# Performance work log

Hardware: AMD Instinct MI355X
Metric: run time of the kernel (lower is better)

Reference implementation:

```python
import jax, jax.numpy as jnp
import numpy as np

SEQ_LEN = 12
BATCH = 2048
IN_DIM = 512
HIDDEN = 1024


def setup_inputs() -> dict:
    key = jax.random.key(0)
    k1, k2, k3, k4 = jax.random.split(key, 4)
    scale = 1.0 / np.sqrt(IN_DIM + HIDDEN)
    return {
        "x": jax.random.normal(k1, (BATCH, SEQ_LEN, IN_DIM), dtype=jnp.float32),
        "coded_cords": jax.random.normal(k2, (BATCH, HIDDEN), dtype=jnp.float32),
        # TF GRUCell fused gate kernel: [in+hidden, 2*hidden] (reset, update), bias init 1.0
        "gate_kernel": jax.random.normal(k3, (IN_DIM + HIDDEN, 2 * HIDDEN), dtype=jnp.float32) * scale,
        "gate_bias": jnp.ones((2 * HIDDEN,), dtype=jnp.float32),
        # candidate kernel: [in+hidden, hidden], zero bias
        "cand_kernel": jax.random.normal(k4, (IN_DIM + HIDDEN, HIDDEN), dtype=jnp.float32) * scale,
        "cand_bias": jnp.zeros((HIDDEN,), dtype=jnp.float32),
    }


def reference(x, coded_cords, gate_kernel, gate_bias, cand_kernel, cand_bias):
    # GRU recurrence (tf.contrib.rnn.GRUCell math), initial state = coded_cords.
    def step(h, xt):
        # xt: [B, D], h: [B, H]
        gates = jax.nn.sigmoid(jnp.concatenate([xt, h], axis=-1) @ gate_kernel + gate_bias)
        r, u = jnp.split(gates, 2, axis=-1)  # reset, update gates [B, H]
        c = jnp.tanh(jnp.concatenate([xt, r * h], axis=-1) @ cand_kernel + cand_bias)
        h_new = u * h + (1.0 - u) * c
        return h_new, h_new

    xs = jnp.swapaxes(x, 0, 1)  # [T, B, D]
    _, ys = jax.lax.scan(step, coded_cords, xs)  # ys: [T, B, H]
    return jnp.swapaxes(ys, 0, 1)  # [B, T, H]
```

## Files before the change

### kernel.cpp

```cpp
#include <hip/hip_runtime.h>
#include <hip/hip_bf16.h>


#define T_SEQ 12
#define BATCH 2048
#define IND 512
#define HID 1024
#define NGATE (2 * HID)
#define NPRE (NGATE + HID)

typedef __bf16 bf16x8 __attribute__((ext_vector_type(8)));
typedef __bf16 bf16x4 __attribute__((ext_vector_type(4)));
typedef float floatx4 __attribute__((ext_vector_type(4)));

#define AS1 __attribute__((address_space(1)))
#define AS3 __attribute__((address_space(3)))

__device__ __forceinline__ void gload16(const __bf16* g, __bf16* l) {
  __builtin_amdgcn_global_load_lds((const AS1 void*)g, (AS3 void*)l, 16, 0, 0);
}

__device__ __forceinline__ float fast_sigmoid(float v) {
  v = fminf(30.f, fmaxf(-30.f, v));
  return 1.f / (1.f + __expf(-v));
}
__device__ __forceinline__ float fast_tanh(float v) {
  v = fminf(15.f, fmaxf(-15.f, v));
  float e = __expf(2.f * v);
  return (e - 1.f) / (e + 1.f);
}

__global__ __launch_bounds__(256) void prep(
    const float* __restrict__ Wg, const float* __restrict__ Wc,
    const float* __restrict__ x, const float* __restrict__ coded,
    __bf16* __restrict__ Bx, __bf16* __restrict__ Bhg, __bf16* __restrict__ Bhc,
    __bf16* __restrict__ xb, float* __restrict__ h32, __bf16* __restrict__ hb) {
  int b = blockIdx.x;
  if (b < 2304) {
    int gid = b * 256 + threadIdx.x;
    int g = gid >> 6, lane = gid & 63;
    const float* W; int ld, row0, ksteps, wid; __bf16* out;
    if (g < 2048)      { W = Wg; ld = NGATE; row0 = 0;   ksteps = 16; wid = g;        out = Bx; }
    else if (g < 3072) { W = Wc; ld = HID;   row0 = 0;   ksteps = 16; wid = g - 2048; out = Bx + (size_t)2048 * 512; }
    else if (g < 7168) { W = Wg; ld = NGATE; row0 = IND; ksteps = 32; wid = g - 3072; out = Bhg; }
    else               { W = Wc; ld = HID;   row0 = IND; ksteps = 32; wid = g - 7168; out = Bhc; }
    int n16 = wid / ksteps, kt = wid - n16 * ksteps;
    int col = n16 * 16 + (lane & 15);
    int k0 = row0 + kt * 32 + (lane >> 4) * 8;
    bf16x8 v;
#pragma unroll
    for (int j = 0; j < 8; ++j) v[j] = (__bf16)W[(size_t)(k0 + j) * ld + col];
    *reinterpret_cast<bf16x8*>(out + (size_t)wid * 512 + lane * 8) = v;
  } else if (b < 4352) {
    int i = (b - 2304) * 256 + threadIdx.x;
    const float4* x4 = (const float4*)x;
    const int n4 = BATCH * T_SEQ * IND / 4;
    for (int k = i; k < n4; k += 2048 * 256) {
      float4 v = x4[k];
      bf16x4 o;
      o[0] = (__bf16)v.x; o[1] = (__bf16)v.y; o[2] = (__bf16)v.z; o[3] = (__bf16)v.w;
      *reinterpret_cast<bf16x4*>(xb + (size_t)k * 4) = o;
    }
  } else {
    int i = (b - 4352) * 256 + threadIdx.x;
    float4 v = ((const float4*)coded)[i];
    ((float4*)h32)[i] = v;
    bf16x4 o;
    o[0] = (__bf16)v.x; o[1] = (__bf16)v.y; o[2] = (__bf16)v.z; o[3] = (__bf16)v.w;
    *reinterpret_cast<bf16x4*>(hb + (size_t)i * 4) = o;
  }
}

__global__ __launch_bounds__(256) void pre_gemm(
    const __bf16* __restrict__ xb, const __bf16* __restrict__ Bx,
    const float* __restrict__ bg, const float* __restrict__ bc,
    __bf16* __restrict__ Pg, __bf16* __restrict__ Pc) {
  __shared__ __bf16 Alds[128 * 64];
  __shared__ __bf16 Blds[8192];
  const int tid = threadIdx.x, lane = tid & 63, w = tid >> 6;
  const int wm = w >> 1, wn = w & 1, quad = lane >> 4, l16 = lane & 15;
  const int bid = blockIdx.x;
  const int wg = (bid & 7) * 576 + (bid >> 3);
  const int nb = wg % 24;
  const int rest = wg / 24;
  const int mB = rest & 15;
  const int tz = rest >> 4;
  const int m0 = mB * 128;

  const __bf16* gA[4]; __bf16* lA[4];
  const __bf16* gB[4]; __bf16* lB[4];
#pragma unroll
  for (int i = 0; i < 4; ++i) {
    int c = tid + i * 256;
    int row = c >> 3, k8 = c & 7;
    gA[i] = xb + ((size_t)(m0 + row) * T_SEQ + tz) * IND + ((k8 ^ (row & 7)) * 8);
    lA[i] = Alds + c * 8;
    int ks2c = c >> 9, rem = c & 511;
    gB[i] = Bx + (((size_t)(nb * 8 + (rem >> 6)) * 16 + ks2c) * 64 + (rem & 63)) * 8;
    lB[i] = Blds + c * 8;
  }

  floatx4 acc[4][4] = {};
  for (int it = 0; it < 8; ++it) {
    __syncthreads();
#pragma unroll
    for (int i = 0; i < 4; ++i) gload16(gA[i] + it * 64, lA[i]);
#pragma unroll
    for (int i = 0; i < 4; ++i) gload16(gB[i] + (size_t)it * 1024, lB[i]);
    __syncthreads();
#pragma unroll
    for (int ks2 = 0; ks2 < 2; ++ks2) {
      bf16x8 af[4], bfr[4];
#pragma unroll
      for (int mf = 0; mf < 4; ++mf) {
        int row = wm * 64 + mf * 16 + l16;
        af[mf] = *(const bf16x8*)&Alds[row * 64 + (((ks2 * 4 + quad) ^ (row & 7)) * 8)];
      }
#pragma unroll
      for (int nf = 0; nf < 4; ++nf)
        bfr[nf] = *(const bf16x8*)&Blds[(ks2 * 512 + (wn * 4 + nf) * 64 + lane) * 8];
#pragma unroll
      for (int mf = 0; mf < 4; ++mf)
#pragma unroll
        for (int nf = 0; nf < 4; ++nf)
          acc[mf][nf] = __builtin_amdgcn_mfma_f32_16x16x32_bf16(af[mf], bfr[nf], acc[mf][nf], 0, 0, 0);
    }
  }

  const int n64g = nb * 2 + wn;
  const bool isg = (n64g < 32);
  __bf16* P = isg ? Pg : Pc;
  const float* bias = isg ? bg : bc;
  const int nrel = isg ? n64g : (n64g - 32);
  const int colb = nrel * 64 + l16;
#pragma unroll
  for (int mf = 0; mf < 4; ++mf) {
    int m32 = mB * 4 + wm * 2 + (mf >> 1);
    size_t tb = isg ? (((size_t)tz * 64 + m32) * 32 + n64g) * 2048
                    : (((size_t)tz * 64 + m32) * 16 + nrel) * 2048;
#pragma unroll
    for (int nf = 0; nf < 4; ++nf) {
      float bv = bias[colb + nf * 16];
      bf16x4 st;
#pragma unroll
      for (int i = 0; i < 4; ++i) st[i] = (__bf16)(acc[mf][nf][i] + bv);
      *(bf16x4*)&P[tb + (size_t)(((mf & 1) * 4 + nf) * 64 + lane) * 4] = st;
    }
  }
}

__global__ __launch_bounds__(256, 2) void gate_step(
    const __bf16* __restrict__ hb, const __bf16* __restrict__ Bhg,
    const __bf16* __restrict__ Pg, _Float16* __restrict__ u16,
    __bf16* __restrict__ rhb, int t) {
  __shared__ __bf16 Alds[64 * 128];
  __shared__ __bf16 Blds[16384];
  const int tid = threadIdx.x, lane = tid & 63, w = tid >> 6;
  const int wm = w >> 1, wn = w & 1, quad = lane >> 4, l16 = lane & 15;
  const int bid = blockIdx.x;
  const int swz = (bid & 7) * 64 + (bid >> 3);
  const int mT = swz & 31, nT = swz >> 5;

  const __bf16* gA[4]; __bf16* lA[4];
  const __bf16* gB[8]; __bf16* lB[8];
#pragma unroll
  for (int i = 0; i < 4; ++i) {
    int c = tid + i * 256;
    int row = c >> 4, ch = c & 15;
    gA[i] = hb + (size_t)(mT * 64 + row) * HID + ((ch ^ (row & 7)) * 8);
    lA[i] = Alds + c * 8;
  }
#pragma unroll
  for (int i = 0; i < 8; ++i) {
    int c = tid + i * 256;
    gB[i] = Bhg + (size_t)(nT * 8 + (c >> 8)) * 16384 + (c & 255) * 8;
    lB[i] = Blds + c * 8;
  }

  floatx4 acc[2][4] = {};
  for (int kt = 0; kt < 8; ++kt) {
    __syncthreads();
#pragma unroll
    for (int i = 0; i < 4; ++i) gload16(gA[i] + kt * 128, lA[i]);
#pragma unroll
    for (int i = 0; i < 8; ++i) gload16(gB[i] + kt * 2048, lB[i]);
    __syncthreads();
#pragma unroll
    for (int ks2 = 0; ks2 < 4; ++ks2) {
      bf16x8 af[2], bfr[4];
#pragma unroll
      for (int mf = 0; mf < 2; ++mf) {
        int row = wm * 32 + mf * 16 + l16;
        af[mf] = *(const bf16x8*)&Alds[row * 128 + (((ks2 * 4 + quad) ^ (row & 7)) * 8)];
      }
#pragma unroll
      for (int nf = 0; nf < 4; ++nf)
        bfr[nf] = *(const bf16x8*)&Blds[(wn * 4 + nf) * 2048 + ks2 * 512 + lane * 8];
#pragma unroll
      for (int mf = 0; mf < 2; ++mf)
#pragma unroll
        for (int nf = 0; nf < 4; ++nf)
          acc[mf][nf] = __builtin_amdgcn_mfma_f32_16x16x32_bf16(af[mf], bfr[nf], acc[mf][nf], 0, 0, 0);
    }
  }

  const int m32 = mT * 2 + wm;
  const int n64 = nT * 2 + wn;
  const bool isr = (n64 < 16);
  size_t tb = (((size_t)t * 64 + m32) * 32 + n64) * 2048;
#pragma unroll
  for (int mf = 0; mf < 2; ++mf)
#pragma unroll
    for (int nf = 0; nf < 4; ++nf) {
      bf16x4 px = *(const bf16x4*)&Pg[tb + (size_t)((mf * 4 + nf) * 64 + lane) * 4];
      int col = nT * 128 + wn * 64 + nf * 16 + l16;
      int rowb = mT * 64 + wm * 32 + mf * 16 + quad * 4;
#pragma unroll
      for (int i = 0; i < 4; ++i) {
        float s = fast_sigmoid(acc[mf][nf][i] + (float)px[i]);
        if (isr) {
          size_t idx = (size_t)(rowb + i) * HID + col;
          rhb[idx] = (__bf16)(s * (float)hb[idx]);
        } else {
          u16[(size_t)(rowb + i) * HID + (col - HID)] = (_Float16)s;
        }
      }
    }
}

__global__ __launch_bounds__(256, 2) void cand_step(
    const __bf16* __restrict__ rhb, const __bf16* __restrict__ Bhc,
    const __bf16* __restrict__ Pc, const _Float16* __restrict__ u16,
    float* __restrict__ h32, __bf16* __restrict__ hb,
    float* __restrict__ out, int t) {
  __shared__ __bf16 Alds[64 * 128];
  __shared__ __bf16 Blds[8192];
  const int tid = threadIdx.x, lane = tid & 63, w = tid >> 6;
  const int wm = w >> 1, wn = w & 1, quad = lane >> 4, l16 = lane & 15;
  const int bid = blockIdx.x;
  const int swz = (bid & 7) * 64 + (bid >> 3);
  const int mT = swz & 31, nT = swz >> 5;

  const __bf16* gA[4]; __bf16* lA[4];
  const __bf16* gB[4]; __bf16* lB[4];
#pragma unroll
  for (int i = 0; i < 4; ++i) {
    int c = tid + i * 256;
    int row = c >> 4, ch = c & 15;
    gA[i] = rhb + (size_t)(mT * 64 + row) * HID + ((ch ^ (row & 7)) * 8);
    lA[i] = Alds + c * 8;
    gB[i] = Bhc + (size_t)(nT * 4 + (c >> 8)) * 16384 + (c & 255) * 8;
    lB[i] = Blds + c * 8;
  }

  floatx4 acc[2][2] = {};
  for (int kt = 0; kt < 8; ++kt) {
    __syncthreads();
#pragma unroll
    for (int i = 0; i < 4; ++i) gload16(gA[i] + kt * 128, lA[i]);
#pragma unroll
    for (int i = 0; i < 4; ++i) gload16(gB[i] + kt * 2048, lB[i]);
    __syncthreads();
#pragma unroll
    for (int ks2 = 0; ks2 < 4; ++ks2) {
      bf16x8 af[2], bfr[2];
#pragma unroll
      for (int mf = 0; mf < 2; ++mf) {
        int row = wm * 32 + mf * 16 + l16;
        af[mf] = *(const bf16x8*)&Alds[row * 128 + (((ks2 * 4 + quad) ^ (row & 7)) * 8)];
      }
#pragma unroll
      for (int nf = 0; nf < 2; ++nf)
        bfr[nf] = *(const bf16x8*)&Blds[(wn * 2 + nf) * 2048 + ks2 * 512 + lane * 8];
#pragma unroll
      for (int mf = 0; mf < 2; ++mf)
#pragma unroll
        for (int nf = 0; nf < 2; ++nf)
          acc[mf][nf] = __builtin_amdgcn_mfma_f32_16x16x32_bf16(af[mf], bfr[nf], acc[mf][nf], 0, 0, 0);
    }
  }

  const int m32 = mT * 2 + wm;
  size_t tb = (((size_t)t * 64 + m32) * 16 + nT) * 2048;
#pragma unroll
  for (int mf = 0; mf < 2; ++mf)
#pragma unroll
    for (int nf = 0; nf < 2; ++nf) {
      bf16x4 px = *(const bf16x4*)&Pc[tb + (size_t)((mf * 4 + wn * 2 + nf) * 64 + lane) * 4];
      int col = nT * 64 + wn * 32 + nf * 16 + l16;
      int rowb = mT * 64 + wm * 32 + mf * 16 + quad * 4;
#pragma unroll
      for (int i = 0; i < 4; ++i) {
        float c = fast_tanh(acc[mf][nf][i] + (float)px[i]);
        size_t idx = (size_t)(rowb + i) * HID + col;
        float u = (float)u16[idx];
        float hnew = u * h32[idx] + (1.f - u) * c;
        h32[idx] = hnew;
        hb[idx] = (__bf16)hnew;
        __builtin_nontemporal_store(hnew, &out[(size_t)(rowb + i) * (T_SEQ * HID) + t * HID + col]);
      }
    }
}

extern "C" void kernel_launch(void* const* d_in, const int* in_sizes, int n_in,
                              void* d_out, int out_size, void* d_ws, size_t ws_size,
                              hipStream_t stream) {
  const float* x     = (const float*)d_in[0];
  const float* coded = (const float*)d_in[1];
  const float* Wg_f  = (const float*)d_in[2];
  const float* bg    = (const float*)d_in[3];
  const float* Wc_f  = (const float*)d_in[4];
  const float* bc    = (const float*)d_in[5];
  float* out = (float*)d_out;

  uintptr_t base = ((uintptr_t)d_ws + 255) & ~(uintptr_t)255;
  auto take = [&](size_t bytes) {
    void* p = (void*)base;
    base = (base + bytes + 255) & ~(uintptr_t)255;
    return p;
  };
  __bf16* Bx  = (__bf16*)take((size_t)(NPRE / 16) * 16 * 512 * 2);
  __bf16* Bhg = (__bf16*)take((size_t)(NGATE / 16) * 32 * 512 * 2);
  __bf16* Bhc = (__bf16*)take((size_t)(HID / 16) * 32 * 512 * 2);
  __bf16* Pg  = (__bf16*)take((size_t)T_SEQ * 64 * 32 * 2048 * 2);
  __bf16* Pc  = (__bf16*)take((size_t)T_SEQ * 64 * 16 * 2048 * 2);
  __bf16* xb  = (__bf16*)take((size_t)BATCH * T_SEQ * IND * 2);
  float*  h32 = (float*) take((size_t)BATCH * HID * 4);
  __bf16* hb  = (__bf16*)take((size_t)BATCH * HID * 2);
  _Float16* u16 = (_Float16*)take((size_t)BATCH * HID * 2);
  __bf16* rhb = (__bf16*)take((size_t)BATCH * HID * 2);

  prep<<<6400, 256, 0, stream>>>(Wg_f, Wc_f, x, coded, Bx, Bhg, Bhc, xb, h32, hb);

  pre_gemm<<<4608, 256, 0, stream>>>(xb, Bx, bg, bc, Pg, Pc);

  for (int t = 0; t < T_SEQ; ++t) {
    gate_step<<<512, 256, 0, stream>>>(hb, Bhg, Pg, u16, rhb, t);
    cand_step<<<512, 256, 0, stream>>>(rhb, Bhc, Pc, u16, h32, hb, out, t);
  }
}
```

Before: 734.9 us.

## Fuse recurrent GRU steps into one persistent kernel with per-row-tile counters

Replaces the 24 per-timestep gate/candidate launches with a single persistent kernel of 512 blocks. Each block handles one batch row tile and one column slice, and blocks sync through atomic counters scoped to the 16 blocks that share that row tile. The gate output columns are remapped so each block owns matching reset and update slices. The update gate stays in LDS instead of round-tripping through global memory, and h values are reused from the loaded A tile. This removes launch overhead and grid-wide barriers. It relies on all 512 blocks being co-resident and on coherent loads (glc) for cross-block visibility with relaxed atomics.

```diff
diff --git a/kernel.cpp b/kernel.cpp
--- a/kernel.cpp
+++ b/kernel.cpp
@@ -19,6 +19,9 @@
 __device__ __forceinline__ void gload16(const __bf16* g, __bf16* l) {
   __builtin_amdgcn_global_load_lds((const AS1 void*)g, (AS3 void*)l, 16, 0, 0);
 }
+__device__ __forceinline__ void gload16c(const __bf16* g, __bf16* l) {
+  __builtin_amdgcn_global_load_lds((const AS1 void*)g, (AS3 void*)l, 16, 0, 1);
+}
 
 __device__ __forceinline__ float fast_sigmoid(float v) {
   v = fminf(30.f, fmaxf(-30.f, v));
@@ -34,7 +37,8 @@
     const float* __restrict__ Wg, const float* __restrict__ Wc,
     const float* __restrict__ x, const float* __restrict__ coded,
     __bf16* __restrict__ Bx, __bf16* __restrict__ Bhg, __bf16* __restrict__ Bhc,
-    __bf16* __restrict__ xb, float* __restrict__ h32, __bf16* __restrict__ hb) {
+    __bf16* __restrict__ xb, float* __restrict__ h32, __bf16* __restrict__ hb,
+    unsigned* __restrict__ ctr) {
   int b = blockIdx.x;
   if (b < 2304) {
     int gid = b * 256 + threadIdx.x;
@@ -63,6 +67,10 @@
     }
   } else {
     int i = (b - 4352) * 256 + threadIdx.x;
+    if (b == 4352) {
+#pragma unroll
+      for (int j = 0; j < 4; ++j) ctr[threadIdx.x + j * 256] = 0u;
+    }
     float4 v = ((const float4*)coded)[i];
     ((float4*)h32)[i] = v;
     bf16x4 o;
@@ -149,157 +157,165 @@
   }
 }
 
-__global__ __launch_bounds__(256, 2) void gate_step(
-    const __bf16* __restrict__ hb, const __bf16* __restrict__ Bhg,
-    const __bf16* __restrict__ Pg, _Float16* __restrict__ u16,
-    __bf16* __restrict__ rhb, int t) {
+__global__ __launch_bounds__(256, 2) void gru_steps(
+    const __bf16* __restrict__ Bhg, const __bf16* __restrict__ Bhc,
+    const __bf16* __restrict__ Pg, const __bf16* __restrict__ Pc,
+    float* __restrict__ h32, __bf16* __restrict__ hb,
+    __bf16* __restrict__ rhb, float* __restrict__ out,
+    unsigned* __restrict__ ctr) {
   __shared__ __bf16 Alds[64 * 128];
   __shared__ __bf16 Blds[16384];
+  float* uS = (float*)&Blds[8192];
   const int tid = threadIdx.x, lane = tid & 63, w = tid >> 6;
   const int wm = w >> 1, wn = w & 1, quad = lane >> 4, l16 = lane & 15;
   const int bid = blockIdx.x;
-  const int swz = (bid & 7) * 64 + (bid >> 3);
-  const int mT = swz & 31, nT = swz >> 5;
-
-  const __bf16* gA[4]; __bf16* lA[4];
-  const __bf16* gB[8]; __bf16* lB[8];
+  const int mT = (bid & 7) * 4 + ((bid >> 3) & 3);
+  const int sub = bid >> 5;
+  unsigned* cG = ctr + mT * 16;
+  unsigned* cC = ctr + 512 + mT * 16;
+
+  int offA[4];
 #pragma unroll
   for (int i = 0; i < 4; ++i) {
-    int c = tid + i * 256;
-    int row = c >> 4, ch = c & 15;
-    gA[i] = hb + (size_t)(mT * 64 + row) * HID + ((ch ^ (row & 7)) * 8);
-    lA[i] = Alds + c * 8;
-  }
-#pragma unroll
-  for (int i = 0; i < 8; ++i) {
-    int c = tid + i * 256;
-    gB[i] = Bhg + (size_t)(nT * 8 + (c >> 8)) * 16384 + (c & 255) * 8;
-    lB[i] = Blds + c * 8;
-  }
-
-  floatx4 acc[2][4] = {};
-  for (int kt = 0; kt < 8; ++kt) {
-    __syncthreads();
-#pragma unroll
-    for (int i = 0; i < 4; ++i) gload16(gA[i] + kt * 128, lA[i]);
-#pragma unroll
-    for (int i = 0; i < 8; ++i) gload16(gB[i] + kt * 2048, lB[i]);
-    __syncthreads();
-#pragma unroll
-    for (int ks2 = 0; ks2 < 4; ++ks2) {
-      bf16x8 af[2], bfr[4];
-#pragma unroll
-      for (int mf = 0; mf < 2; ++mf) {
-        int row = wm * 32 + mf * 16 + l16;
-        af[mf] = *(const bf16x8*)&Alds[row * 128 + (((ks2 * 4 + quad) ^ (row & 7)) * 8)];
+    int c = tid + i * 256, row = c >> 4, ch = c & 15;
+    offA[i] = (mT * 64 + row) * HID + ((ch ^ (row & 7)) * 8);
+  }
+
+  for (int t = 0; t < T_SEQ; ++t) {
+    {
+      floatx4 acc[2][4] = {};
+      __bf16 hr[2][4][4];
+      for (int kt = 0; kt < 8; ++kt) {
+        __syncthreads();
+#pragma unroll
+        for (int i = 0; i < 4; ++i)
+          gload16c(hb + offA[i] + kt * 128, Alds + (tid + i * 256) * 8);
+#pragma unroll
+        for (int i = 0; i < 8; ++i) {
+          int gidx = (i < 4) ? (sub * 4 + i) : (64 + sub * 4 + (i - 4));
+          gload16(Bhg + (size_t)gidx * 16384 + kt * 2048 + tid * 8,
+                  Blds + (tid + i * 256) * 8);
+        }
+        __syncthreads();
+#pragma unroll
+        for (int ks2 = 0; ks2 < 4; ++ks2) {
+          bf16x8 af[2], bfr[4];
+#pragma unroll
+          for (int mf = 0; mf < 2; ++mf) {
+            int row = wm * 32 + mf * 16 + l16;
+            af[mf] = *(const bf16x8*)&Alds[row * 128 + (((ks2 * 4 + quad) ^ (row & 7)) * 8)];
+          }
+#pragma unroll
+          for (int nf = 0; nf < 4; ++nf)
+            bfr[nf] = *(const bf16x8*)&Blds[(wn * 4 + nf) * 2048 + ks2 * 512 + lane * 8];
+#pragma unroll
+          for (int mf = 0; mf < 2; ++mf)
+#pragma unroll
+            for (int nf = 0; nf < 4; ++nf)
+              acc[mf][nf] = __builtin_amdgcn_mfma_f32_16x16x32_bf16(af[mf], bfr[nf], acc[mf][nf], 0, 0, 0);
+        }
+        if (kt == (sub >> 1) && wn == 0) {
+#pragma unroll
+          for (int mf = 0; mf < 2; ++mf)
+#pragma unroll
+            for (int nf = 0; nf < 4; ++nf)
+#pragma unroll
+              for (int i = 0; i < 4; ++i) {
+                int r = wm * 32 + mf * 16 + quad * 4 + i;
+                int c = (sub & 1) * 64 + nf * 16 + l16;
+                hr[mf][nf][i] = Alds[r * 128 + (((c >> 3) ^ (r & 7)) * 8) + (c & 7)];
+              }
+        }
       }
-#pragma unroll
-      for (int nf = 0; nf < 4; ++nf)
-        bfr[nf] = *(const bf16x8*)&Blds[(wn * 4 + nf) * 2048 + ks2 * 512 + lane * 8];
+      const int n64 = wn * 16 + sub;
+      const int m32 = mT * 2 + wm;
+      size_t tb = (((size_t)t * 64 + m32) * 32 + n64) * 2048;
 #pragma unroll
       for (int mf = 0; mf < 2; ++mf)
 #pragma unroll
-        for (int nf = 0; nf < 4; ++nf)
-          acc[mf][nf] = __builtin_amdgcn_mfma_f32_16x16x32_bf16(af[mf], bfr[nf], acc[mf][nf], 0, 0, 0);
-    }
-  }
-
-  const int m32 = mT * 2 + wm;
-  const int n64 = nT * 2 + wn;
-  const bool isr = (n64 < 16);
-  size_t tb = (((size_t)t * 64 + m32) * 32 + n64) * 2048;
-#pragma unroll
-  for (int mf = 0; mf < 2; ++mf)
-#pragma unroll
-    for (int nf = 0; nf < 4; ++nf) {
-      bf16x4 px = *(const bf16x4*)&Pg[tb + (size_t)((mf * 4 + nf) * 64 + lane) * 4];
-      int col = nT * 128 + wn * 64 + nf * 16 + l16;
-      int rowb = mT * 64 + wm * 32 + mf * 16 + quad * 4;
-#pragma unroll
-      for (int i = 0; i < 4; ++i) {
-        float s = fast_sigmoid(acc[mf][nf][i] + (float)px[i]);
-        if (isr) {
-          size_t idx = (size_t)(rowb + i) * HID + col;
-          rhb[idx] = (__bf16)(s * (float)hb[idx]);
-        } else {
-          u16[(size_t)(rowb + i) * HID + (col - HID)] = (_Float16)s;
+        for (int nf = 0; nf < 4; ++nf) {
+          bf16x4 px = *(const bf16x4*)&Pg[tb + (size_t)((mf * 4 + nf) * 64 + lane) * 4];
+          int rowb = mT * 64 + wm * 32 + mf * 16 + quad * 4;
+#pragma unroll
+          for (int i = 0; i < 4; ++i) {
+            float s = fast_sigmoid(acc[mf][nf][i] + (float)px[i]);
+            if (wn == 0) {
+              rhb[(size_t)(rowb + i) * HID + sub * 64 + nf * 16 + l16] =
+                  (__bf16)(s * (float)hr[mf][nf][i]);
+            } else {
+              uS[(wm * 32 + mf * 16 + quad * 4 + i) * 64 + nf * 16 + l16] = s;
+            }
+          }
+        }
+    }
+    __syncthreads();
+    if (tid == 0) {
+      __hip_atomic_fetch_add(cG, 1u, __ATOMIC_RELAXED, __HIP_MEMORY_SCOPE_AGENT);
+      unsigned tgt = 16u * (t + 1);
+      while (__hip_atomic_load(cG, __ATOMIC_RELAXED, __HIP_MEMORY_SCOPE_AGENT) < tgt)
+        __builtin_amdgcn_s_sleep(2);
+    }
+    __syncthreads();
+    {
+      floatx4 acc[2][2] = {};
+      for (int kt = 0; kt < 8; ++kt) {
+        __syncthreads();
+#pragma unroll
+        for (int i = 0; i < 4; ++i)
+          gload16c(rhb + offA[i] + kt * 128, Alds + (tid + i * 256) * 8);
+#pragma unroll
+        for (int i = 0; i < 4; ++i)
+          gload16(Bhc + (size_t)(sub * 4 + i) * 16384 + kt * 2048 + tid * 8,
+                  Blds + (tid + i * 256) * 8);
+        __syncthreads();
+#pragma unroll
+        for (int ks2 = 0; ks2 < 4; ++ks2) {
+          bf16x8 af[2], bfr[2];
+#pragma unroll
+          for (int mf = 0; mf < 2; ++mf) {
+            int row = wm * 32 + mf * 16 + l16;
+            af[mf] = *(const bf16x8*)&Alds[row * 128 + (((ks2 * 4 + quad) ^ (row & 7)) * 8)];
+          }
+#pragma unroll
+          for (int nf = 0; nf < 2; ++nf)
+            bfr[nf] = *(const bf16x8*)&Blds[(wn * 2 + nf) * 2048 + ks2 * 512 + lane * 8];
+#pragma unroll
+          for (int mf = 0; mf < 2; ++mf)
+#pragma unroll
+            for (int nf = 0; nf < 2; ++nf)
+              acc[mf][nf] = __builtin_amdgcn_mfma_f32_16x16x32_bf16(af[mf], bfr[nf], acc[mf][nf], 0, 0, 0);
         }
       }
-    }
-}
-
-__global__ __launch_bounds__(256, 2) void cand_step(
-    const __bf16* __restrict__ rhb, const __bf16* __restrict__ Bhc,
-    const __bf16* __restrict__ Pc, const _Float16* __restrict__ u16,
-    float* __restrict__ h32, __bf16* __restrict__ hb,
-    float* __restrict__ out, int t) {
-  __shared__ __bf16 Alds[64 * 128];
-  __shared__ __bf16 Blds[8192];
-  const int tid = threadIdx.x, lane = tid & 63, w = tid >> 6;
-  const int wm = w >> 1, wn = w & 1, quad = lane >> 4, l16 = lane & 15;
-  const int bid = blockIdx.x;
-  const int swz = (bid & 7) * 64 + (bid >> 3);
-  const int mT = swz & 31, nT = swz >> 5;
-
-  const __bf16* gA[4]; __bf16* lA[4];
-  const __bf16* gB[4]; __bf16* lB[4];
-#pragma unroll
-  for (int i = 0; i < 4; ++i) {
-    int c = tid + i * 256;
-    int row = c >> 4, ch = c & 15;
-    gA[i] = rhb + (size_t)(mT * 64 + row) * HID + ((ch ^ (row & 7)) * 8);
-    lA[i] = Alds + c * 8;
-    gB[i] = Bhc + (size_t)(nT * 4 + (c >> 8)) * 16384 + (c & 255) * 8;
-    lB[i] = Blds + c * 8;
-  }
-
-  floatx4 acc[2][2] = {};
-  for (int kt = 0; kt < 8; ++kt) {
-    __syncthreads();
-#pragma unroll
-    for (int i = 0; i < 4; ++i) gload16(gA[i] + kt * 128, lA[i]);
-#pragma unroll
-    for (int i = 0; i < 4; ++i) gload16(gB[i] + kt * 2048, lB[i]);
-    __syncthreads();
-#pragma unroll
-    for (int ks2 = 0; ks2 < 4; ++ks2) {
-      bf16x8 af[2], bfr[2];
-#pragma unroll
-      for (int mf = 0; mf < 2; ++mf) {
-        int row = wm * 32 + mf * 16 + l16;
-        af[mf] = *(const bf16x8*)&Alds[row * 128 + (((ks2 * 4 + quad) ^ (row & 7)) * 8)];
-      }
-#pragma unroll
-      for (int nf = 0; nf < 2; ++nf)
-        bfr[nf] = *(const bf16x8*)&Blds[(wn * 2 + nf) * 2048 + ks2 * 512 + lane * 8];
+      const int m32 = mT * 2 + wm;
+      size_t tb = (((size_t)t * 64 + m32) * 16 + sub) * 2048;
 #pragma unroll
       for (int mf = 0; mf < 2; ++mf)
 #pragma unroll
-        for (int nf = 0; nf < 2; ++nf)
-          acc[mf][nf] = __builtin_amdgcn_mfma_f32_16x16x32_bf16(af[mf], bfr[nf], acc[mf][nf], 0, 0, 0);
-    }
-  }
-
-  const int m32 = mT * 2 + wm;
-  size_t tb = (((size_t)t * 64 + m32) * 16 + nT) * 2048;
-#pragma unroll
-  for (int mf = 0; mf < 2; ++mf)
-#pragma unroll
-    for (int nf = 0; nf < 2; ++nf) {
-      bf16x4 px = *(const bf16x4*)&Pc[tb + (size_t)((mf * 4 + wn * 2 + nf) * 64 + lane) * 4];
-      int col = nT * 64 + wn * 32 + nf * 16 + l16;
-      int rowb = mT * 64 + wm * 32 + mf * 16 + quad * 4;
-#pragma unroll
-      for (int i = 0; i < 4; ++i) {
-        float c = fast_tanh(acc[mf][nf][i] + (float)px[i]);
-        size_t idx = (size_t)(rowb + i) * HID + col;
-        float u = (float)u16[idx];
-        float hnew = u * h32[idx] + (1.f - u) * c;
-        h32[idx] = hnew;
-        hb[idx] = (__bf16)hnew;
-        __builtin_nontemporal_store(hnew, &out[(size_t)(rowb + i) * (T_SEQ * HID) + t * HID + col]);
-      }
-    }
+        for (int nf = 0; nf < 2; ++nf) {
+          bf16x4 px = *(const bf16x4*)&Pc[tb + (size_t)((mf * 4 + wn * 2 + nf) * 64 + lane) * 4];
+          int col = sub * 64 + wn * 32 + nf * 16 + l16;
+          int rowb = mT * 64 + wm * 32 + mf * 16 + quad * 4;
+#pragma unroll
+          for (int i = 0; i < 4; ++i) {
+            float c = fast_tanh(acc[mf][nf][i] + (float)px[i]);
+            size_t idx = (size_t)(rowb + i) * HID + col;
+            float u = uS[(wm * 32 + mf * 16 + quad * 4 + i) * 64 + wn * 32 + nf * 16 + l16];
+            float hnew = u * h32[idx] + (1.f - u) * c;
+            h32[idx] = hnew;
+            hb[idx] = (__bf16)hnew;
+            __builtin_nontemporal_store(hnew, &out[(size_t)(rowb + i) * (T_SEQ * HID) + t * HID + col]);
+          }
+        }
+    }
+    __syncthreads();
+    if (tid == 0) {
+      __hip_atomic_fetch_add(cC, 1u, __ATOMIC_RELAXED, __HIP_MEMORY_SCOPE_AGENT);
+      unsigned tgt = 16u * (t + 1);
+      while (__hip_atomic_load(cC, __ATOMIC_RELAXED, __HIP_MEMORY_SCOPE_AGENT) < tgt)
+        __builtin_amdgcn_s_sleep(2);
+    }
+    __syncthreads();
+  }
 }
 
 extern "C" void kernel_launch(void* const* d_in, const int* in_sizes, int n_in,
@@ -327,15 +343,12 @@
   __bf16* xb  = (__bf16*)take((size_t)BATCH * T_SEQ * IND * 2);
   float*  h32 = (float*) take((size_t)BATCH * HID * 4);
   __bf16* hb  = (__bf16*)take((size_t)BATCH * HID * 2);
-  _Float16* u16 = (_Float16*)take((size_t)BATCH * HID * 2);
   __bf16* rhb = (__bf16*)take((size_t)BATCH * HID * 2);
-
-  prep<<<6400, 256, 0, stream>>>(Wg_f, Wc_f, x, coded, Bx, Bhg, Bhc, xb, h32, hb);
+  unsigned* ctr = (unsigned*)take(1024 * sizeof(unsigned));
+
+  prep<<<6400, 256, 0, stream>>>(Wg_f, Wc_f, x, coded, Bx, Bhg, Bhc, xb, h32, hb, ctr);
 
   pre_gemm<<<4608, 256, 0, stream>>>(xb, Bx, bg, bc, Pg, Pc);
 
-  for (int t = 0; t < T_SEQ; ++t) {
-    gate_step<<<512, 256, 0, stream>>>(hb, Bhg, Pg, u16, rhb, t);
-    cand_step<<<512, 256, 0, stream>>>(rhb, Bhc, Pc, u16, h32, hb, out, t);
-  }
-}
+  gru_steps<<<512, 256, 0, stream>>>(Bhg, Bhc, Pg, Pc, h32, hb, rhb, out, ctr);
+}
```

Result: faster. 716.8 us (-2.5%).
